# Kernel tuning notes

Measured on AMD Instinct MI355X. Metric: run time of the kernel, lower is better.

## Reference

```python
import jax, jax.numpy as jnp
import numpy as np

K = 16  # neighbors per node (knn_graph, loop=False)


def setup_inputs() -> dict:
    key = jax.random.key(0)
    ks = jax.random.split(key, 4)
    B, N = 32, 2048
    coords = jax.random.normal(ks[0], (B, N, 3), jnp.float32)

    def lin(k, i, o):  # glorot-ish init
        return jax.random.normal(k, (i, o), jnp.float32) / np.sqrt(i).astype(np.float32)

    return {
        "coords": coords,
        "W1": lin(ks[1], 3, 64),   "b1": jnp.zeros((64,), jnp.float32),
        "W2": lin(ks[2], 64, 128), "b2": jnp.zeros((128,), jnp.float32),
        "Wf": lin(ks[3], 128, 128), "bf": jnp.zeros((128,), jnp.float32),
    }


def _knn_idx(c, k):
    # c: [N,3] -> [N,k] indices of k nearest neighbors (self excluded, loop=False)
    n = c.shape[0]
    d2 = jnp.sum((c[:, None, :] - c[None, :, :]) ** 2, axis=-1)  # [N,N]
    d2 = jnp.where(jnp.eye(n, dtype=bool), jnp.inf, d2)
    _, idx = jax.lax.top_k(-d2, k)  # smallest distances
    return idx


def _gcn(x, nbr_self, W, b):
    # PyG GCNConv with add_self_loops: every node has in-degree exactly k+1
    # (k knn edges + self-loop), so the symmetric gcn_norm
    # 1/sqrt(deg_i*deg_j) reduces to the constant 1/(k+1).
    h = x @ W                                   # [N,out]
    agg = h[nbr_self].sum(axis=1) / nbr_self.shape[1]
    return agg + b


def reference(coords, W1, b1, W2, b2, Wf, bf):
    n = coords.shape[1]

    def per_sample(c):
        nbr = _knn_idx(c, K)                                     # [N,K]
        nbr_self = jnp.concatenate([nbr, jnp.arange(n)[:, None]], axis=1)  # [N,K+1]
        x = jax.nn.relu(_gcn(c, nbr_self, W1, b1))
        x = jax.nn.relu(_gcn(x, nbr_self, W2, b2))
        return x @ Wf + bf                                       # [N,128]

    return jax.vmap(per_sample)(coords)  # [B,N,128]
```

## Files before the change

kernel.cpp:

```cpp
#include <hip/hip_runtime.h>
#include <hip/hip_bf16.h>

typedef unsigned int u32;
typedef __attribute__((ext_vector_type(8))) short bf16x8;
typedef __attribute__((ext_vector_type(4))) float f32x4;

#define N_NODES 2048
#define INF __builtin_inff()

__device__ __forceinline__ float bflo(u32 u){ return __uint_as_float(u << 16); }
__device__ __forceinline__ float bfhi(u32 u){ return __uint_as_float(u & 0xFFFF0000u); }
__device__ __forceinline__ u32 packbf(float a, float b){
  u32 ua = __float_as_uint(a), ub = __float_as_uint(b);
  u32 ra = (ua + 0x7FFFu + ((ua >> 16) & 1u)) >> 16;
  u32 rb = (ub + 0x7FFFu + ((ub >> 16) & 1u)) >> 16;
  return ra | (rb << 16);
}

__device__ __forceinline__ float dist2(float cx, float cy, float cz,
                                       float jx, float jy, float jz) {
  float dx = cx - jx, dy = cy - jy, dz = cz - jz;
  return fmaf(dz, dz, fmaf(dy, dy, dx * dx));
}

__device__ __forceinline__ float mkkey(float d, int j, int node) {
  u32 kb = (__float_as_uint(d) & 0xFFFFF800u) | (u32)j;
  if (j == node) kb = 0x7E000000u;
  return __uint_as_float(kb);
}

__device__ __forceinline__ void ins8(float (&ad)[8], float v) {
#pragma unroll
  for (int t = 7; t >= 1; --t)
    ad[t] = __builtin_amdgcn_fmed3f(v, ad[t-1], ad[t]);
  ad[0] = fminf(ad[0], v);
}
__device__ __forceinline__ void ins16(float (&ad)[16], float v) {
#pragma unroll
  for (int t = 15; t >= 1; --t)
    ad[t] = __builtin_amdgcn_fmed3f(v, ad[t-1], ad[t]);
  ad[0] = fminf(ad[0], v);
}

__device__ __forceinline__ void merge8s(float (&ad)[16], int tid) {
#define CED(I, J) { float lo_ = fminf(ad[I], ad[J]); ad[J] = fmaxf(ad[I], ad[J]); ad[I] = lo_; }
#define CLEAN16 \
  CED(0,8) CED(1,9) CED(2,10) CED(3,11) CED(4,12) CED(5,13) CED(6,14) CED(7,15) \
  CED(0,4) CED(1,5) CED(2,6)  CED(3,7)  CED(8,12) CED(9,13) CED(10,14) CED(11,15) \
  CED(0,2) CED(1,3) CED(4,6)  CED(5,7)  CED(8,10) CED(9,11) CED(12,14) CED(13,15) \
  CED(0,1) CED(2,3) CED(4,5)  CED(6,7)  CED(8,9)  CED(10,11) CED(12,13) CED(14,15)
  float bd[16];
#pragma unroll
  for (int q = 0; q < 16; ++q) bd[q] = __shfl(ad[q], tid ^ 1);
#pragma unroll
  for (int q = 0; q < 16; ++q) ad[q] = fminf(ad[q], bd[15 - q]);
  CLEAN16
#pragma unroll
  for (int q = 0; q < 16; ++q) bd[q] = __shfl(ad[q], tid ^ 2);
#pragma unroll
  for (int q = 0; q < 16; ++q) ad[q] = fminf(ad[q], bd[15 - q]);
  CLEAN16
#pragma unroll
  for (int q = 0; q < 16; ++q) bd[q] = __shfl(ad[q], tid ^ 4);
#pragma unroll
  for (int q = 0; q < 16; ++q) ad[q] = fminf(ad[q], bd[15 - q]);
  CLEAN16
#undef CLEAN16
#undef CED
}

__device__ __forceinline__ bool node_try8(
    const float (&ad)[8], int tid, int sub, int& j0, int& j1)
{
  const float myMax = ad[7];
  float md[16];
#pragma unroll
  for (int q = 0; q < 8; ++q) md[q] = ad[q];
#pragma unroll
  for (int q = 8; q < 16; ++q) md[q] = __uint_as_float(0x7F000000u);
  merge8s(md, tid);
  const float md15 = md[15];
  float mnext = INF;
#pragma unroll
  for (int q = 7; q >= 0; --q) mnext = (ad[q] > md15) ? ad[q] : mnext;
  float cand17 = fminf(mnext, __shfl(mnext, tid ^ 1));
  cand17 = fminf(cand17, __shfl(cand17, tid ^ 2));
  cand17 = fminf(cand17, __shfl(cand17, tid ^ 4));
  const u32 t15 = __float_as_uint(md15)   & 0xFFFFF800u;
  const u32 t17 = __float_as_uint(cand17) & 0xFFFFF800u;
  j0 = (int)(__float_as_uint(md[(sub<<1)+0]) & 0x7FFu);
  j1 = (int)(__float_as_uint(md[(sub<<1)+1]) & 0x7FFu);
  return (myMax >= cand17) && (t17 >= t15 + 0x800u);
}

__device__ __forceinline__ void node_fb8(
    int node, int tid, int sub, int ln,
    float cx, float cy, float cz, const float* __restrict__ cs,
    u32 (*nbuf)[16], u32* ncnt, int& j0, int& j1)
{
  float a3[16];
#pragma unroll
  for (int q = 0; q < 16; ++q) a3[q] = INF;
#pragma unroll 1
  for (int it = 0; it < 64; ++it) {
    const int v4 = (it << 3) + sub;
    const float4* p = (const float4*)(cs + v4 * 12);
    float4 p0 = p[0], p1 = p[1], p2 = p[2];
    const int base = v4 << 2;
    float d0 = (base + 0 == node) ? INF : dist2(cx,cy,cz, p0.x,p0.y,p0.z);
    float d1 = (base + 1 == node) ? INF : dist2(cx,cy,cz, p0.w,p1.x,p1.y);
    float d2 = (base + 2 == node) ? INF : dist2(cx,cy,cz, p1.z,p1.w,p2.x);
    float d3 = (base + 3 == node) ? INF : dist2(cx,cy,cz, p2.y,p2.z,p2.w);
    ins16(a3, d0); ins16(a3, d1); ins16(a3, d2); ins16(a3, d3);
  }
  merge8s(a3, tid);
  const float tau = a3[15];
  if (sub == 0) ncnt[ln] = 0;
  asm volatile("s_waitcnt lgkmcnt(0)" ::: "memory");
#pragma unroll 1
  for (int it = 0; it < 64; ++it) {
    const int v4 = (it << 3) + sub;
    const float4* p = (const float4*)(cs + v4 * 12);
    float4 p0 = p[0], p1 = p[1], p2 = p[2];
    const int base = v4 << 2;
    float d0 = dist2(cx,cy,cz, p0.x,p0.y,p0.z);
    float d1 = dist2(cx,cy,cz, p0.w,p1.x,p1.y);
    float d2 = dist2(cx,cy,cz, p1.z,p1.w,p2.x);
    float d3 = dist2(cx,cy,cz, p2.y,p2.z,p2.w);
    if (d0 <= tau && base + 0 != node) { u32 p_ = atomicAdd(&ncnt[ln], 1u); if (p_ < 16u) nbuf[ln][p_] = (u32)(base + 0); }
    if (d1 <= tau && base + 1 != node) { u32 p_ = atomicAdd(&ncnt[ln], 1u); if (p_ < 16u) nbuf[ln][p_] = (u32)(base + 1); }
    if (d2 <= tau && base + 2 != node) { u32 p_ = atomicAdd(&ncnt[ln], 1u); if (p_ < 16u) nbuf[ln][p_] = (u32)(base + 2); }
    if (d3 <= tau && base + 3 != node) { u32 p_ = atomicAdd(&ncnt[ln], 1u); if (p_ < 16u) nbuf[ln][p_] = (u32)(base + 3); }
  }
  asm volatile("s_waitcnt lgkmcnt(0)" ::: "memory");
  j0 = (int)nbuf[ln][(sub << 1) + 0];
  j1 = (int)nbuf[ln][(sub << 1) + 1];
}

__global__ __launch_bounds__(256) void k1_knn_l1(
    const float* __restrict__ coords, const float* __restrict__ W1,
    const float* __restrict__ b1, int* __restrict__ nbr, u32* __restrict__ x1)
{
  __shared__ u32   nbuf[32][16];
  __shared__ u32   ncnt[32];
  __shared__ float w1s[192];
  __shared__ float b1s[64];
  const int tid   = threadIdx.x;
  const int s     = blockIdx.x >> 6;
  const int chunk = blockIdx.x & 63;
  const float* cs = coords + (size_t)s * (N_NODES * 3);
  if (tid < 192) w1s[tid] = W1[tid];
  if (tid < 64)  b1s[tid] = b1[tid];
  __syncthreads();

  const int ln   = tid >> 3;
  const int sub  = tid & 7;
  const int node = (chunk << 5) + ln;
  const float cx = cs[3*node], cy = cs[3*node+1], cz = cs[3*node+2];

  float ad[8];
#pragma unroll
  for (int q = 0; q < 8; ++q) ad[q] = INF;

  for (int it = 0; it < 32; ++it) {
    const int v4a = (it << 4) + sub, v4b = v4a + 8;
    const float4* pa = (const float4*)(cs + v4a * 12);
    const float4* pb = (const float4*)(cs + v4b * 12);
    float4 a0 = pa[0], a1 = pa[1], a2 = pa[2];
    float4 b0 = pb[0], b1v = pb[1], b2 = pb[2];
    const int ba = v4a << 2, bb = v4b << 2;
    ins8(ad, mkkey(dist2(cx,cy,cz, a0.x,a0.y,a0.z),   ba+0, node));
    ins8(ad, mkkey(dist2(cx,cy,cz, a0.w,a1.x,a1.y),   ba+1, node));
    ins8(ad, mkkey(dist2(cx,cy,cz, a1.z,a1.w,a2.x),   ba+2, node));
    ins8(ad, mkkey(dist2(cx,cy,cz, a2.y,a2.z,a2.w),   ba+3, node));
    ins8(ad, mkkey(dist2(cx,cy,cz, b0.x,b0.y,b0.z),   bb+0, node));
    ins8(ad, mkkey(dist2(cx,cy,cz, b0.w,b1v.x,b1v.y), bb+1, node));
    ins8(ad, mkkey(dist2(cx,cy,cz, b1v.z,b1v.w,b2.x), bb+2, node));
    ins8(ad, mkkey(dist2(cx,cy,cz, b2.y,b2.z,b2.w),   bb+3, node));
  }

  int j0, j1;
  const bool ok = node_try8(ad, tid, sub, j0, j1);
  if (!__all((int)ok)) {
    node_fb8(node, tid, sub, ln, cx, cy, cz, cs, nbuf, ncnt, j0, j1);
  }

  const size_t gnode = ((size_t)s << 11) + node;
  *(int2*)(nbr + gnode * 16 + (sub << 1)) = make_int2(j0, j1);

  float sx, sy, sz;
  if (sub == 0) { sx = cx; sy = cy; sz = cz; } else { sx = 0.f; sy = 0.f; sz = 0.f; }
  sx += cs[3*j0]   + cs[3*j1];
  sy += cs[3*j0+1] + cs[3*j1+1];
  sz += cs[3*j0+2] + cs[3*j1+2];
  sx += __shfl_xor(sx, 1); sx += __shfl_xor(sx, 2); sx += __shfl_xor(sx, 4);
  sy += __shfl_xor(sy, 1); sy += __shfl_xor(sy, 2); sy += __shfl_xor(sy, 4);
  sz += __shfl_xor(sz, 1); sz += __shfl_xor(sz, 2); sz += __shfl_xor(sz, 4);
  const float inv = 1.0f / 17.0f;
  float mx = sx * inv, my = sy * inv, mz = sz * inv;

  u32 pk[4];
#pragma unroll
  for (int oo = 0; oo < 8; oo += 2) {
    const int o = (sub << 3) + oo;
    float v0 = fmaf(mz, w1s[128+o],   fmaf(my, w1s[64+o],   fmaf(mx, w1s[o],   b1s[o])));
    float v1 = fmaf(mz, w1s[128+o+1], fmaf(my, w1s[64+o+1], fmaf(mx, w1s[o+1], b1s[o+1])));
    pk[oo >> 1] = packbf(fmaxf(v0, 0.0f), fmaxf(v1, 0.0f));
  }
  *(uint4*)(x1 + gnode * 32 + (sub << 2)) = make_uint4(pk[0], pk[1], pk[2], pk[3]);
}

__global__ __launch_bounds__(256) void k2_gcn2(
    const u32* __restrict__ x1, const int* __restrict__ nbr,
    const float* __restrict__ W2, const float* __restrict__ b2,
    u32* __restrict__ x2)
{
  __shared__ uint4 AldsV[1024];
  __shared__ uint4 BhiV[1024];
  __shared__ uint4 BloV[1024];
  char* Alds = (char*)AldsV; char* Bhi = (char*)BhiV; char* Blo = (char*)BloV;
  const int tid   = threadIdx.x;
  const int node0 = blockIdx.x << 7;

#pragma unroll
  for (int i = 0; i < 32; ++i) {
    int e = tid + (i << 8);
    int k = e >> 7, n = e & 127;
    float w = W2[e];
    u32 hb = packbf(w, 0.0f) & 0xFFFFu;
    float whi = __uint_as_float(hb << 16);
    u32 lb = packbf(w - whi, 0.0f) & 0xFFFFu;
    int byte = n * 128 + ((2 * k) ^ ((n & 7) << 4));
    *(unsigned short*)(Bhi + byte) = (unsigned short)hb;
    *(unsigned short*)(Blo + byte) = (unsigned short)lb;
  }

  {
    const int r = tid >> 1, half = tid & 1;
    const size_t gnode = (size_t)node0 + r;
    const u32* selfp = x1 + gnode * 32 + half * 16;
    const u32* x1s   = x1 + ((gnode >> 11) << 11) * 32;
    const int* nb    = nbr + gnode * 16;
    float a[32];
#pragma unroll
    for (int q = 0; q < 4; ++q) {
      uint4 v = *(const uint4*)(selfp + (q << 2));
      a[8*q+0] = bflo(v.x); a[8*q+1] = bfhi(v.x);
      a[8*q+2] = bflo(v.y); a[8*q+3] = bfhi(v.y);
      a[8*q+4] = bflo(v.z); a[8*q+5] = bfhi(v.z);
      a[8*q+6] = bflo(v.w); a[8*q+7] = bfhi(v.w);
    }
#pragma unroll
    for (int t = 0; t < 16; ++t) {
      const u32* rp = x1s + (size_t)nb[t] * 32 + half * 16;
#pragma unroll
      for (int q = 0; q < 4; ++q) {
        uint4 v = *(const uint4*)(rp + (q << 2));
        a[8*q+0] += bflo(v.x); a[8*q+1] += bfhi(v.x);
        a[8*q+2] += bflo(v.y); a[8*q+3] += bfhi(v.y);
        a[8*q+4] += bflo(v.z); a[8*q+5] += bfhi(v.z);
        a[8*q+6] += bflo(v.w); a[8*q+7] += bfhi(v.w);
      }
    }
    const float inv = 1.0f / 17.0f;
    u32 pk[16];
#pragma unroll
    for (int j = 0; j < 16; ++j)
      pk[j] = packbf(a[2*j] * inv, a[2*j+1] * inv);
#pragma unroll
    for (int q = 0; q < 4; ++q) {
      int byte = r * 128 + ((((half << 6) + (q << 4))) ^ ((r & 7) << 4));
      *(uint4*)(Alds + byte) = make_uint4(pk[4*q], pk[4*q+1], pk[4*q+2], pk[4*q+3]);
    }
  }
  __syncthreads();

  const int lane = tid & 63, wv = tid >> 6;
  const int cl = lane & 15, kg = lane >> 4;

  f32x4 acc[2][8];
#pragma unroll
  for (int rt = 0; rt < 2; ++rt)
#pragma unroll
    for (int ct = 0; ct < 8; ++ct) {
      float bv = b2[(ct << 4) + cl];
      acc[rt][ct] = (f32x4){bv, bv, bv, bv};
    }

#pragma unroll
  for (int ks = 0; ks < 2; ++ks) {
    const int kb = (ks << 6) + (kg << 4);
    bf16x8 af[2];
#pragma unroll
    for (int rt = 0; rt < 2; ++rt) {
      int row = (wv << 5) + (rt << 4) + cl;
      af[rt] = *(const bf16x8*)(Alds + row * 128 + (kb ^ ((row & 7) << 4)));
    }
#pragma unroll
    for (int ct = 0; ct < 8; ++ct) {
      int n = (ct << 4) + cl;
      int byte = n * 128 + (kb ^ ((n & 7) << 4));
      bf16x8 bh = *(const bf16x8*)(Bhi + byte);
      bf16x8 bl = *(const bf16x8*)(Blo + byte);
#pragma unroll
      for (int rt = 0; rt < 2; ++rt) {
        acc[rt][ct] = __builtin_amdgcn_mfma_f32_16x16x32_bf16(af[rt], bh, acc[rt][ct], 0, 0, 0);
        acc[rt][ct] = __builtin_amdgcn_mfma_f32_16x16x32_bf16(af[rt], bl, acc[rt][ct], 0, 0, 0);
      }
    }
  }

  unsigned short* x2h = (unsigned short*)x2;
#pragma unroll
  for (int rt = 0; rt < 2; ++rt)
#pragma unroll
    for (int ct = 0; ct < 8; ++ct) {
      int colg = (ct << 4) + cl;
      int nr0  = node0 + (wv << 5) + (rt << 4) + (kg << 2);
#pragma unroll
      for (int r = 0; r < 4; ++r) {
        float v = fmaxf(acc[rt][ct][r], 0.0f);
        x2h[(size_t)(nr0 + r) * 128 + colg] = (unsigned short)(packbf(v, 0.0f) & 0xFFFFu);
      }
    }
}

__global__ __launch_bounds__(256) void k3_final(
    const u32* __restrict__ x2, const float* __restrict__ Wf,
    const float* __restrict__ bfv, float* __restrict__ out)
{
  __shared__ uint4 AldsV[2048];
  __shared__ uint4 BhiV[1024];
  __shared__ uint4 BloV[1024];
  char* Alds = (char*)AldsV; char* Bhi = (char*)BhiV; char* Blo = (char*)BloV;
  const int tid   = threadIdx.x;
  const int node0 = (blockIdx.x >> 1) << 7;
  const int ch0   = (blockIdx.x & 1) << 6;

#pragma unroll
  for (int i = 0; i < 32; ++i) {
    int e = tid + (i << 8);
    int k = e >> 6, n = e & 63;
    float w = Wf[k * 128 + ch0 + n];
    u32 hb = packbf(w, 0.0f) & 0xFFFFu;
    float whi = __uint_as_float(hb << 16);
    u32 lb = packbf(w - whi, 0.0f) & 0xFFFFu;
    int byte = n * 256 + ((2 * k) ^ ((n & 15) << 4));
    *(unsigned short*)(Bhi + byte) = (unsigned short)hb;
    *(unsigned short*)(Blo + byte) = (unsigned short)lb;
  }

  {
    const int r = tid >> 1, half = tid & 1;
    const u32* src = x2 + (size_t)(node0 + r) * 64 + half * 32;
#pragma unroll
    for (int q = 0; q < 8; ++q) {
      uint4 v = *(const uint4*)(src + (q << 2));
      int byte = r * 256 + ((((half << 7) + (q << 4))) ^ ((r & 15) << 4));
      *(uint4*)(Alds + byte) = v;
    }
  }
  __syncthreads();

  const int lane = tid & 63, wv = tid >> 6;
  const int cl = lane & 15, kg = lane >> 4;

  f32x4 acc[2][4];
#pragma unroll
  for (int rt = 0; rt < 2; ++rt)
#pragma unroll
    for (int ct = 0; ct < 4; ++ct) {
      float bv = bfv[ch0 + (ct << 4) + cl];
      acc[rt][ct] = (f32x4){bv, bv, bv, bv};
    }

#pragma unroll
  for (int ks = 0; ks < 4; ++ks) {
    const int kb = (ks << 6) + (kg << 4);
    bf16x8 af[2];
#pragma unroll
    for (int rt = 0; rt < 2; ++rt) {
      int row = (wv << 5) + (rt << 4) + cl;
      af[rt] = *(const bf16x8*)(Alds + row * 256 + (kb ^ ((row & 15) << 4)));
    }
#pragma unroll
    for (int ct = 0; ct < 4; ++ct) {
      int n = (ct << 4) + cl;
      int byte = n * 256 + (kb ^ ((n & 15) << 4));
      bf16x8 bh = *(const bf16x8*)(Bhi + byte);
      bf16x8 bl = *(const bf16x8*)(Blo + byte);
#pragma unroll
      for (int rt = 0; rt < 2; ++rt) {
        acc[rt][ct] = __builtin_amdgcn_mfma_f32_16x16x32_bf16(af[rt], bh, acc[rt][ct], 0, 0, 0);
        acc[rt][ct] = __builtin_amdgcn_mfma_f32_16x16x32_bf16(af[rt], bl, acc[rt][ct], 0, 0, 0);
      }
    }
  }

#pragma unroll
  for (int rt = 0; rt < 2; ++rt)
#pragma unroll
    for (int ct = 0; ct < 4; ++ct) {
      int col = ch0 + (ct << 4) + cl;
      int nr0 = node0 + (wv << 5) + (rt << 4) + (kg << 2);
#pragma unroll
      for (int r = 0; r < 4; ++r)
        out[(size_t)(nr0 + r) * 128 + col] = acc[rt][ct][r];
    }
}

extern "C" void kernel_launch(void* const* d_in, const int* in_sizes, int n_in,
                              void* d_out, int out_size, void* d_ws, size_t ws_size,
                              hipStream_t stream) {
  const float* coords = (const float*)d_in[0];
  const float* W1 = (const float*)d_in[1];
  const float* b1 = (const float*)d_in[2];
  const float* W2 = (const float*)d_in[3];
  const float* b2 = (const float*)d_in[4];
  const float* Wf = (const float*)d_in[5];
  const float* bf = (const float*)d_in[6];
  float* out = (float*)d_out;

  char* ws = (char*)d_ws;
  int* nbr = (int*)ws;
  u32* x1  = (u32*)(ws + (size_t)4  * 1024 * 1024);
  u32* x2  = (u32*)(ws + (size_t)12 * 1024 * 1024);

  k1_knn_l1<<<2048, 256, 0, stream>>>(coords, W1, b1, nbr, x1);
  k2_gcn2  <<< 512, 256, 0, stream>>>(x1, nbr, W2, b2, x2);
  k3_final <<<1024, 256, 0, stream>>>(x2, Wf, bf, out);
}
```

Baseline: 172.2 us.

## Drop self-exclusion in kNN scan and software-pipeline coordinate loads

The kNN scan no longer masks the self node per candidate. The node itself, at distance zero, is allowed into the top list and then replaced in slot 0 by the 17th candidate, with the exactness check shifted to the 17th and 18th keys. The scan loop is also double-buffered, prefetching the next iteration's coordinates into a second register set while the current ones are processed. This removes a compare and select per candidate and hides load latency, at the cost of extra registers and one more shuffle-reduction round. It assumes the self node always ranks first, which duplicate coordinates could break.

```diff
diff --git a/kernel.cpp b/kernel.cpp
--- a/kernel.cpp
+++ b/kernel.cpp
@@ -23,10 +23,8 @@
   return fmaf(dz, dz, fmaf(dy, dy, dx * dx));
 }
 
-__device__ __forceinline__ float mkkey(float d, int j, int node) {
-  u32 kb = (__float_as_uint(d) & 0xFFFFF800u) | (u32)j;
-  if (j == node) kb = 0x7E000000u;
-  return __uint_as_float(kb);
+__device__ __forceinline__ float mkk(float d, int j) {
+  return __uint_as_float((__float_as_uint(d) & 0xFFFFF800u) | (u32)j);
 }
 
 __device__ __forceinline__ void ins8(float (&ad)[8], float v) {
@@ -83,14 +81,21 @@
   float mnext = INF;
 #pragma unroll
   for (int q = 7; q >= 0; --q) mnext = (ad[q] > md15) ? ad[q] : mnext;
-  float cand17 = fminf(mnext, __shfl(mnext, tid ^ 1));
-  cand17 = fminf(cand17, __shfl(cand17, tid ^ 2));
-  cand17 = fminf(cand17, __shfl(cand17, tid ^ 4));
-  const u32 t15 = __float_as_uint(md15)   & 0xFFFFF800u;
-  const u32 t17 = __float_as_uint(cand17) & 0xFFFFF800u;
+  float c17 = fminf(mnext, __shfl(mnext, tid ^ 1));
+  c17 = fminf(c17, __shfl(c17, tid ^ 2));
+  c17 = fminf(c17, __shfl(c17, tid ^ 4));
+  float mnext2 = INF;
+#pragma unroll
+  for (int q = 7; q >= 0; --q) mnext2 = (ad[q] > c17) ? ad[q] : mnext2;
+  float c18 = fminf(mnext2, __shfl(mnext2, tid ^ 1));
+  c18 = fminf(c18, __shfl(c18, tid ^ 2));
+  c18 = fminf(c18, __shfl(c18, tid ^ 4));
+  const u32 t17 = __float_as_uint(c17) & 0xFFFFF800u;
+  const u32 t18 = __float_as_uint(c18) & 0xFFFFF800u;
+  md[0] = c17;
   j0 = (int)(__float_as_uint(md[(sub<<1)+0]) & 0x7FFu);
   j1 = (int)(__float_as_uint(md[(sub<<1)+1]) & 0x7FFu);
-  return (myMax >= cand17) && (t17 >= t15 + 0x800u);
+  return (myMax >= c18) && (t18 >= t17 + 0x800u);
 }
 
 __device__ __forceinline__ void node_fb8(
@@ -162,22 +167,37 @@
 #pragma unroll
   for (int q = 0; q < 8; ++q) ad[q] = INF;
 
-  for (int it = 0; it < 32; ++it) {
-    const int v4a = (it << 4) + sub, v4b = v4a + 8;
-    const float4* pa = (const float4*)(cs + v4a * 12);
-    const float4* pb = (const float4*)(cs + v4b * 12);
-    float4 a0 = pa[0], a1 = pa[1], a2 = pa[2];
-    float4 b0 = pb[0], b1v = pb[1], b2 = pb[2];
-    const int ba = v4a << 2, bb = v4b << 2;
-    ins8(ad, mkkey(dist2(cx,cy,cz, a0.x,a0.y,a0.z),   ba+0, node));
-    ins8(ad, mkkey(dist2(cx,cy,cz, a0.w,a1.x,a1.y),   ba+1, node));
-    ins8(ad, mkkey(dist2(cx,cy,cz, a1.z,a1.w,a2.x),   ba+2, node));
-    ins8(ad, mkkey(dist2(cx,cy,cz, a2.y,a2.z,a2.w),   ba+3, node));
-    ins8(ad, mkkey(dist2(cx,cy,cz, b0.x,b0.y,b0.z),   bb+0, node));
-    ins8(ad, mkkey(dist2(cx,cy,cz, b0.w,b1v.x,b1v.y), bb+1, node));
-    ins8(ad, mkkey(dist2(cx,cy,cz, b1v.z,b1v.w,b2.x), bb+2, node));
-    ins8(ad, mkkey(dist2(cx,cy,cz, b2.y,b2.z,b2.w),   bb+3, node));
-  }
+#define LOAD6(P0,P1,P2,P3,P4,P5, ITV) {                                   \
+    const int v4a_ = ((ITV) << 4) + sub;                                  \
+    const float4* pa_ = (const float4*)(cs + v4a_ * 12);                  \
+    const float4* pb_ = (const float4*)(cs + (v4a_ + 8) * 12);            \
+    P0 = pa_[0]; P1 = pa_[1]; P2 = pa_[2];                                \
+    P3 = pb_[0]; P4 = pb_[1]; P5 = pb_[2]; }
+
+#define BODY(P0,P1,P2,P3,P4,P5, ITV) {                                    \
+    const int ba_ = (((ITV) << 4) + sub) << 2, bb_ = ba_ + 32;            \
+    ins8(ad, mkk(dist2(cx,cy,cz, P0.x,P0.y,P0.z),   ba_+0));              \
+    ins8(ad, mkk(dist2(cx,cy,cz, P0.w,P1.x,P1.y),   ba_+1));              \
+    ins8(ad, mkk(dist2(cx,cy,cz, P1.z,P1.w,P2.x),   ba_+2));              \
+    ins8(ad, mkk(dist2(cx,cy,cz, P2.y,P2.z,P2.w),   ba_+3));              \
+    ins8(ad, mkk(dist2(cx,cy,cz, P3.x,P3.y,P3.z),   bb_+0));              \
+    ins8(ad, mkk(dist2(cx,cy,cz, P3.w,P4.x,P4.y),   bb_+1));              \
+    ins8(ad, mkk(dist2(cx,cy,cz, P4.z,P4.w,P5.x),   bb_+2));              \
+    ins8(ad, mkk(dist2(cx,cy,cz, P5.y,P5.z,P5.w),   bb_+3)); }
+
+  {
+    float4 A0, A1, A2, A3, A4, A5, B0, B1, B2, B3, B4, B5;
+    LOAD6(A0,A1,A2,A3,A4,A5, 0)
+#pragma unroll 1
+    for (int it = 0; it < 32; it += 2) {
+      LOAD6(B0,B1,B2,B3,B4,B5, it + 1)
+      BODY (A0,A1,A2,A3,A4,A5, it)
+      LOAD6(A0,A1,A2,A3,A4,A5, (it + 2) & 31)
+      BODY (B0,B1,B2,B3,B4,B5, it + 1)
+    }
+  }
+#undef LOAD6
+#undef BODY
 
   int j0, j1;
   const bool ok = node_try8(ad, tid, sub, j0, j1);
```

Result: faster. 166.3 us (-3.4%).
